# Kernel optimization log

Measured on AMD Instinct MI355X. Metric: run time of the kernel, lower is better.

## Reference

```python
import jax, jax.numpy as jnp
import numpy as np


def setup_inputs() -> dict:
    key = jax.random.key(0)
    ks = jax.random.split(key, 18)
    B, T, L, C = 16, 512, 50, 7
    H = 512
    s = 0.05
    inp = {
        "phone_data": jax.random.normal(ks[0], (B, T, L, C), jnp.float32),
        "h0": jax.random.normal(ks[1], (B, H), jnp.float32),
        "conv1_w": jax.random.normal(ks[2], (128, 7, 11), jnp.float32) * s,
        "conv1_b": jax.random.normal(ks[3], (128,), jnp.float32) * s,
        "conv2_w": jax.random.normal(ks[4], (256, 128, 9), jnp.float32) * s,
        "conv2_b": jax.random.normal(ks[5], (256,), jnp.float32) * s,
        "fc1_w": jax.random.normal(ks[6], (1024, 1536), jnp.float32) * s,
        "fc1_b": jax.random.normal(ks[7], (1024,), jnp.float32) * s,
        "fc2_w": jax.random.normal(ks[8], (512, 1024), jnp.float32) * s,
        "fc2_b": jax.random.normal(ks[9], (512,), jnp.float32) * s,
        "gru_wih": jax.random.normal(ks[10], (3 * H, H), jnp.float32) * s,
        "gru_whh": jax.random.normal(ks[11], (3 * H, H), jnp.float32) * s,
        "gru_bih": jax.random.normal(ks[12], (3 * H,), jnp.float32) * s,
        "gru_bhh": jax.random.normal(ks[13], (3 * H,), jnp.float32) * s,
        "fc3_w": jax.random.normal(ks[14], (1, H), jnp.float32) * s,
        "fc3_b": jax.random.normal(ks[15], (1,), jnp.float32) * s,
    }
    return inp


def reference(phone_data, h0, conv1_w, conv1_b, conv2_w, conv2_b,
              fc1_w, fc1_b, fc2_w, fc2_b,
              gru_wih, gru_whh, gru_bih, gru_bhh, fc3_w, fc3_b):
    B, T, L, C = phone_data.shape
    N = B * T
    # ---- batched CNN + FC feature extractor (independent per frame) ----
    x = phone_data.reshape(N, L, C).transpose(0, 2, 1)  # [N, 7, 50]
    y = jax.lax.conv_general_dilated(
        x, conv1_w, (1,), 'VALID',
        dimension_numbers=('NCH', 'OIH', 'NCH')) + conv1_b[None, :, None]  # [N,128,40]
    y = y.reshape(N, 128, 20, 2).max(-1)  # maxpool k=2,s=2 -> [N,128,20]
    y = jax.lax.conv_general_dilated(
        y, conv2_w, (1,), 'VALID',
        dimension_numbers=('NCH', 'OIH', 'NCH')) + conv2_b[None, :, None]  # [N,256,12]
    y = y.reshape(N, 256, 6, 2).max(-1)  # [N,256,6]
    feat = y.reshape(N, 1536)            # Flatten(0): channel-major, matches torch
    feat = feat @ fc1_w.T + fc1_b        # [N,1024]
    feat = feat @ fc2_w.T + fc2_b        # [N,512]
    feat = feat.reshape(B, T, 512)

    # ---- sequential GRUCell recurrence (PyTorch GRUCell math) ----
    def cell(h, x_t):
        gi = x_t @ gru_wih.T + gru_bih   # [B, 3H]
        gh = h @ gru_whh.T + gru_bhh     # [B, 3H]
        ir, iz, in_ = jnp.split(gi, 3, axis=-1)
        hr, hz, hn = jnp.split(gh, 3, axis=-1)
        r = jax.nn.sigmoid(ir + hr)
        z = jax.nn.sigmoid(iz + hz)
        n = jnp.tanh(in_ + r * hn)
        h_new = (1 - z) * n + z * h
        # original code calls hx.detach() every step
        h_new = jax.lax.stop_gradient(h_new)
        return h_new, h_new

    _, hs = jax.lax.scan(cell, h0, feat.transpose(1, 0, 2))  # hs: [T,B,512]
    out = hs @ fc3_w.T + fc3_b  # [T,B,1]
    return out.transpose(1, 0, 2)  # [B,T,1]
```

## Files before the change

### kernel.cpp

```cpp
#include <hip/hip_runtime.h>
#include <hip/hip_bf16.h>
#include <math.h>
#include <stdint.h>

typedef __attribute__((ext_vector_type(8))) short short8;
typedef __attribute__((ext_vector_type(4))) float f32x4;
typedef __attribute__((ext_vector_type(4))) unsigned int uint4v;

#define T_ 512

__device__ __forceinline__ unsigned short bf16rn(float f) {
  union { float f; unsigned u; } x; x.f = f;
  unsigned r = x.u + 0x7FFF + ((x.u >> 16) & 1);
  return (unsigned short)(r >> 16);
}

__device__ __forceinline__ void gload16(const void* gsrc, void* ldst) {
  __builtin_amdgcn_global_load_lds(
      (const __attribute__((address_space(1))) unsigned int*)gsrc,
      (__attribute__((address_space(3))) unsigned int*)ldst, 16, 0, 0);
}

__device__ __forceinline__ void wg_barrier() {
  __builtin_amdgcn_sched_barrier(0);
  asm volatile("s_waitcnt lgkmcnt(0)" ::: "memory");
  __builtin_amdgcn_sched_barrier(0);
  __builtin_amdgcn_s_barrier();
  __builtin_amdgcn_sched_barrier(0);
}

__global__ __launch_bounds__(256) void conv1_kernel(
    const float* __restrict__ phone, const float* __restrict__ w1,
    const float* __restrict__ b1, ushort* __restrict__ out1b) {
  __shared__ float ws[128 * 77];
  __shared__ float bs[128];
  __shared__ float xs[8][7][52];
  const int tid = threadIdx.x;
  const int n0 = blockIdx.x * 8;
  for (int idx = tid; idx < 9856; idx += 256) ws[idx] = w1[idx];
  if (tid < 128) bs[tid] = b1[tid];
  for (int idx = tid; idx < 2800; idx += 256) {
    int fi = idx / 350, r = idx - fi * 350;
    int ll = r / 7, c = r - ll * 7;
    xs[fi][c][ll] = phone[(size_t)(n0 + fi) * 350 + r];
  }
  __syncthreads();

  const int o = tid >> 1, ph = tid & 1;
  const float* wo = ws + o * 77;
  const float bb = bs[o];
  for (int fi = 0; fi < 8; ++fi) {
    float acc0[10], acc1[10];
#pragma unroll
    for (int q = 0; q < 10; ++q) { acc0[q] = 0.f; acc1[q] = 0.f; }
    for (int i = 0; i < 7; ++i) {
      float wr[11];
#pragma unroll
      for (int k = 0; k < 11; ++k) wr[k] = wo[i * 11 + k];
#pragma unroll
      for (int q = 0; q < 10; ++q) {
        int p = ph * 10 + q;
        int base = 2 * p;
        float xv[12];
#pragma unroll
        for (int j = 0; j < 12; ++j) xv[j] = xs[fi][i][base + j];
        float s0 = 0.f, s1 = 0.f;
#pragma unroll
        for (int k = 0; k < 11; ++k) {
          s0 += xv[k] * wr[k];
          s1 += xv[k + 1] * wr[k];
        }
        acc0[q] += s0;
        acc1[q] += s1;
      }
    }
#pragma unroll
    for (int q = 0; q < 10; ++q) {
      int p = ph * 10 + q;
      out1b[((size_t)(n0 + fi) * 128 + o) * 20 + p] =
          bf16rn(fmaxf(acc0[q], acc1[q]) + bb);
    }
  }
}

__global__ __launch_bounds__(256) void f32_to_bf16(
    const float* __restrict__ src, ushort* __restrict__ dst, int n4) {
  int i = blockIdx.x * 256 + threadIdx.x;
  if (i < n4) {
    float4 v = ((const float4*)src)[i];
    ushort4 o;
    o.x = bf16rn(v.x); o.y = bf16rn(v.y); o.z = bf16rn(v.z); o.w = bf16rn(v.w);
    ((ushort4*)dst)[i] = o;
  }
}

__global__ __launch_bounds__(256) void stage_h0(
    const float* __restrict__ h0, unsigned long long* __restrict__ hxt) {
  const int tid = threadIdx.x;
  const int b = tid >> 4, x = tid & 15;
#pragma unroll
  for (int q = 0; q < 16; ++q) {
    int d = (x + q * 16) * 2;
    int s = d >> 5, fqq = (d >> 3) & 3, k = (d & 7) >> 1;
    int lane = b | (fqq << 4);
    float2 h2 = *(const float2*)(h0 + (size_t)b * 512 + d);
    unsigned pk = (unsigned)bf16rn(h2.x) | ((unsigned)bf16rn(h2.y) << 16);
    hxt[((size_t)s * 64 + lane) * 4 + k] = (unsigned long long)pk;
  }
}

template <int AM, int EM>
__global__ __launch_bounds__(256) void gemm_bf16(
    const ushort* __restrict__ A, const ushort* __restrict__ W,
    const float* __restrict__ bias, void* __restrict__ Cout,
    int K, int lda, int ldc) {
  __shared__ ushort As[128 * 64];
  __shared__ ushort Bs[128 * 64];
  __shared__ ushort tbl[1152];
  const int tid = threadIdx.x;
  const int l = tid & 63, wv = tid >> 6;
  const int wr = wv >> 1, wc = wv & 1;
  const int fr = l & 15, fq = l >> 4;
  const int bm0 = blockIdx.x * 128, bn0 = blockIdx.y * 128;

  if (AM == 1) {
    for (int idx = tid; idx < 1152; idx += 256) {
      int i2 = idx / 9, kp = idx - i2 * 9;
      tbl[idx] = (ushort)(i2 * 20 + kp);
    }
    __syncthreads();
  }

  f32x4 acc[4][4];
#pragma unroll
  for (int mi = 0; mi < 4; ++mi)
#pragma unroll
    for (int ni = 0; ni < 4; ++ni) acc[mi][ni] = (f32x4)0.f;

  const int pr8 = l >> 3;
  const int pc = l & 7;
  const int nkt = K >> 6;
  for (int kt = 0; kt < nkt; ++kt) {
    const int k0 = kt << 6;
#pragma unroll
    for (int i = 0; i < 4; ++i) {
      int q = wv * 4 + i;
      int prow = q * 8 + pr8;
      int lc = pc ^ (prow & 7);
      gload16(W + (size_t)(bn0 + prow) * K + k0 + lc * 8, &Bs[q * 512]);
    }
    if (AM == 0) {
#pragma unroll
      for (int i = 0; i < 4; ++i) {
        int q = wv * 4 + i;
        int prow = q * 8 + pr8;
        int lc = pc ^ (prow & 7);
        gload16(A + (size_t)(bm0 + prow) * lda + k0 + lc * 8, &As[q * 512]);
      }
    } else {
#pragma unroll
      for (int q = 0; q < 16; ++q) {
        int idx = tid + q * 256;
        int row = idx >> 5, c0 = (idx & 31) * 2;
        int m = bm0 + row;
        int n = m / 12, pos = m - n * 12;
        int kk = k0 + c0;
        const ushort* an = A + (size_t)n * 2560 + pos;
        uint e0 = an[tbl[kk]];
        uint e1 = an[tbl[kk + 1]];
        *(uint*)&As[row * 64 + (((c0 >> 3) ^ (row & 7)) << 3) + (c0 & 7)] =
            e0 | (e1 << 16);
      }
    }
    __syncthreads();
#pragma unroll
    for (int ks = 0; ks < 2; ++ks) {
      short8 af[4], bfr[4];
#pragma unroll
      for (int mi = 0; mi < 4; ++mi) {
        int row = wr * 64 + mi * 16 + fr;
        af[mi] = *(const short8*)&As[row * 64 + (((ks * 4 + fq) ^ (row & 7)) << 3)];
      }
#pragma unroll
      for (int ni = 0; ni < 4; ++ni) {
        int row = wc * 64 + ni * 16 + fr;
        bfr[ni] = *(const short8*)&Bs[row * 64 + (((ks * 4 + fq) ^ (row & 7)) << 3)];
      }
#pragma unroll
      for (int mi = 0; mi < 4; ++mi)
#pragma unroll
        for (int ni = 0; ni < 4; ++ni)
          acc[mi][ni] = __builtin_amdgcn_mfma_f32_16x16x32_bf16(
              af[mi], bfr[ni], acc[mi][ni], 0, 0, 0);
    }
    __syncthreads();
  }

#pragma unroll
  for (int ni = 0; ni < 4; ++ni) {
    int col = bn0 + wc * 64 + ni * 16 + fr;
    float bv = bias[col];
#pragma unroll
    for (int mi = 0; mi < 4; ++mi) {
      int mbase = bm0 + wr * 64 + mi * 16 + fq * 4;
      if (EM == 0) {
        ushort* C = (ushort*)Cout;
#pragma unroll
        for (int j = 0; j < 4; ++j)
          C[(size_t)(mbase + j) * ldc + col] = bf16rn(acc[mi][ni][j] + bv);
      } else if (EM == 1) {
        ushort* C = (ushort*)Cout;
#pragma unroll
        for (int j = 0; j < 4; j += 2) {
          int m = mbase + j;
          int n = m / 12, pos = m - n * 12;
          float v = fmaxf(acc[mi][ni][j], acc[mi][ni][j + 1]) + bv;
          C[(size_t)n * 1536 + col * 6 + (pos >> 1)] = bf16rn(v);
        }
      } else {
        float* C = (float*)Cout;
#pragma unroll
        for (int j = 0; j < 4; ++j) {
          int m = mbase + j;
          int b = m >> 9, tt = m & 511;
          C[((size_t)tt * 16 + b) * 1536 + col] = acc[mi][ni][j] + bv;
        }
      }
    }
  }
}

__global__ __launch_bounds__(384) void gru_persistent(
    const float* __restrict__ h0, const float* __restrict__ gi,
    const float* __restrict__ whh, const float* __restrict__ bhh,
    float* __restrict__ hsbuf, unsigned long long* __restrict__ hxt) {
  __shared__ float gh_lds[6 * 256];
  __shared__ unsigned afl[16 * 64 * 4];
  const int tid = threadIdx.x;
  const int w = blockIdx.x;
  const int l = tid & 63, v = tid >> 6;
  const int fr = l & 15, fq = l >> 4;
  const int g = v >> 1, half = v & 1;
  const int o = g * 512 + w * 32 + half * 16 + fr;

  short8 bfrag[16];
#pragma unroll
  for (int s = 0; s < 16; ++s) {
    const float* wp = whh + (size_t)o * 512 + s * 32 + fq * 8;
    float4 w0 = *(const float4*)wp;
    float4 w1 = *(const float4*)(wp + 4);
    short8 bb;
    bb[0] = (short)bf16rn(w0.x); bb[1] = (short)bf16rn(w0.y);
    bb[2] = (short)bf16rn(w0.z); bb[3] = (short)bf16rn(w0.w);
    bb[4] = (short)bf16rn(w1.x); bb[5] = (short)bf16rn(w1.y);
    bb[6] = (short)bf16rn(w1.z); bb[7] = (short)bf16rn(w1.w);
    bfrag[s] = bb;
  }
  const float bo = bhh[o];

  const int b = tid >> 4, jp = tid & 15, jl = jp * 2;
  const bool gthr = (tid < 256);
  const int pt = tid - 256;
  float hA = 0.f, hB = 0.f;
  float giC0 = 0.f, giC1 = 0.f, giC2 = 0.f, giC3 = 0.f, giC4 = 0.f, giC5 = 0.f;
  float giN0 = 0.f, giN1 = 0.f, giN2 = 0.f, giN3 = 0.f, giN4 = 0.f, giN5 = 0.f;
  if (gthr) {
    float2 h2 = *(const float2*)(h0 + (size_t)b * 512 + w * 32 + jl);
    hA = h2.x; hB = h2.y;
    const float* g0 = gi + (size_t)b * 1536 + w * 32 + jl;
    float2 r0 = *(const float2*)(g0);
    float2 r1 = *(const float2*)(g0 + 512);
    float2 r2 = *(const float2*)(g0 + 1024);
    giC0 = r0.x; giC3 = r0.y; giC1 = r1.x; giC4 = r1.y; giC2 = r2.x; giC5 = r2.y;
    const float* g1 = gi + (size_t)(16 + b) * 1536 + w * 32 + jl;
    float2 s0 = *(const float2*)(g1);
    float2 s1 = *(const float2*)(g1 + 512);
    float2 s2 = *(const float2*)(g1 + 1024);
    giN0 = s0.x; giN3 = s0.y; giN1 = s1.x; giN4 = s1.y; giN2 = s2.x; giN5 = s2.y;
  }

  if (!gthr) {
    const unsigned long long* base = hxt + pt * 2;
    uint4v r[16];
    for (;;) {
#pragma unroll
      for (int m = 0; m < 16; ++m)
        asm volatile("global_load_dwordx4 %0, %1, off sc0 sc1"
                     : "=v"(r[m]) : "v"(base + m * 256));
      asm volatile("s_waitcnt vmcnt(0)" ::: "memory");
      __builtin_amdgcn_sched_barrier(0);
      bool ok = true;
#pragma unroll
      for (int m = 0; m < 16; ++m)
        ok = ok & (r[m].y == 0u) & (r[m].w == 0u);
      if (ok) break;
    }
#pragma unroll
    for (int m = 0; m < 16; ++m)
      *(uint2*)&afl[pt * 2 + m * 256] = make_uint2(r[m].x, r[m].z);
  }
  wg_barrier();

  for (int t = 0; t < T_; ++t) {
    f32x4 a0 = (f32x4)0.f, a1 = (f32x4)0.f, a2 = (f32x4)0.f, a3 = (f32x4)0.f;
#pragma unroll
    for (int s = 0; s < 4; ++s) {
      union { uint4v u; short8 s8; } c0, c1, c2, c3;
      c0.u = *(const uint4v*)&afl[((4 * s + 0) * 64 + l) * 4];
      c1.u = *(const uint4v*)&afl[((4 * s + 1) * 64 + l) * 4];
      c2.u = *(const uint4v*)&afl[((4 * s + 2) * 64 + l) * 4];
      c3.u = *(const uint4v*)&afl[((4 * s + 3) * 64 + l) * 4];
      a0 = __builtin_amdgcn_mfma_f32_16x16x32_bf16(c0.s8, bfrag[4 * s + 0], a0, 0, 0, 0);
      a1 = __builtin_amdgcn_mfma_f32_16x16x32_bf16(c1.s8, bfrag[4 * s + 1], a1, 0, 0, 0);
      a2 = __builtin_amdgcn_mfma_f32_16x16x32_bf16(c2.s8, bfrag[4 * s + 2], a2, 0, 0, 0);
      a3 = __builtin_amdgcn_mfma_f32_16x16x32_bf16(c3.s8, bfrag[4 * s + 3], a3, 0, 0, 0);
    }
#pragma unroll
    for (int j = 0; j < 4; ++j)
      gh_lds[v * 256 + (fq * 4 + j) * 16 + fr] = a0[j] + a1[j] + a2[j] + a3[j] + bo;
    wg_barrier();

    if (gthr) {
      const int hh = jl >> 4, c = jl & 15;
      float2 rr = *(const float2*)&gh_lds[(0 + hh) * 256 + b * 16 + c];
      float2 zz = *(const float2*)&gh_lds[(2 + hh) * 256 + b * 16 + c];
      float2 nn = *(const float2*)&gh_lds[(4 + hh) * 256 + b * 16 + c];
      float rgA = __builtin_amdgcn_rcpf(1.f + __expf(-(giC0 + rr.x)));
      float rgB = __builtin_amdgcn_rcpf(1.f + __expf(-(giC3 + rr.y)));
      float zgA = __builtin_amdgcn_rcpf(1.f + __expf(-(giC1 + zz.x)));
      float zgB = __builtin_amdgcn_rcpf(1.f + __expf(-(giC4 + zz.y)));
      float eA = __expf(2.f * (giC2 + rgA * nn.x));
      float eB = __expf(2.f * (giC5 + rgB * nn.y));
      float ngA = 1.f - 2.f * __builtin_amdgcn_rcpf(eA + 1.f);
      float ngB = 1.f - 2.f * __builtin_amdgcn_rcpf(eB + 1.f);
      hA = (1.f - zgA) * ngA + zgA * hA;
      hB = (1.f - zgB) * ngB + zgB * hB;
      if (t + 1 < T_) {
        unsigned pk = (unsigned)bf16rn(hA) | ((unsigned)bf16rn(hB) << 16);
        unsigned long long payload =
            (unsigned long long)pk | ((unsigned long long)(unsigned)(t + 1) << 32);
        unsigned long long* dst =
            hxt + (((size_t)((t + 1) & 1) * 16 + w) * 64 + (b | ((jp >> 2) << 4))) * 4 +
            (jp & 3);
        __hip_atomic_store(dst, payload, __ATOMIC_RELAXED, __HIP_MEMORY_SCOPE_AGENT);
      }
      *(float2*)(hsbuf + ((size_t)t * 16 + b) * 512 + w * 32 + jl) =
          make_float2(hA, hB);
      giC0 = giN0; giC1 = giN1; giC2 = giN2;
      giC3 = giN3; giC4 = giN4; giC5 = giN5;
      if (t + 2 < T_) {
        const float* gb = gi + ((size_t)(t + 2) * 16 + b) * 1536 + w * 32 + jl;
        float2 r0 = *(const float2*)(gb);
        float2 r1 = *(const float2*)(gb + 512);
        float2 r2 = *(const float2*)(gb + 1024);
        giN0 = r0.x; giN3 = r0.y; giN1 = r1.x; giN4 = r1.y; giN2 = r2.x; giN5 = r2.y;
      }
    } else if (t + 1 < T_) {
      const unsigned long long* base =
          hxt + (size_t)((t + 1) & 1) * 4096 + pt * 2;
      const unsigned tag = (unsigned)(t + 1);
      uint4v r[16];
      for (;;) {
#pragma unroll
        for (int m = 0; m < 16; ++m)
          asm volatile("global_load_dwordx4 %0, %1, off sc0 sc1"
                       : "=v"(r[m]) : "v"(base + m * 256));
        asm volatile("s_waitcnt vmcnt(0)" ::: "memory");
        __builtin_amdgcn_sched_barrier(0);
        bool ok = true;
#pragma unroll
        for (int m = 0; m < 16; ++m)
          ok = ok & (r[m].y == tag) & (r[m].w == tag);
        if (ok) break;
      }
#pragma unroll
      for (int m = 0; m < 16; ++m)
        *(uint2*)&afl[pt * 2 + m * 256] = make_uint2(r[m].x, r[m].z);
    }
    wg_barrier();
  }
}

__global__ __launch_bounds__(256) void fc3_kernel(
    const float* __restrict__ hs, const float* __restrict__ w3,
    const float* __restrict__ b3, float* __restrict__ out) {
  __shared__ float w[512];
  const int tid = threadIdx.x;
  w[tid] = w3[tid];
  w[tid + 256] = w3[tid + 256];
  __syncthreads();
  const int gidx = blockIdx.x * 256 + tid;
  const int b = gidx >> 9, t = gidx & 511;
  const float4* hr = (const float4*)(hs + ((size_t)t * 16 + b) * 512);
  const float4* wr = (const float4*)w;
  float acc = 0.f;
#pragma unroll 8
  for (int kc = 0; kc < 128; ++kc) {
    float4 h = hr[kc], ww = wr[kc];
    acc += h.x * ww.x + h.y * ww.y + h.z * ww.z + h.w * ww.w;
  }
  out[gidx] = acc + b3[0];
}

extern "C" void kernel_launch(void* const* d_in, const int* in_sizes, int n_in,
                              void* d_out, int out_size, void* d_ws,
                              size_t ws_size, hipStream_t stream) {
  const float* phone = (const float*)d_in[0];
  const float* h0    = (const float*)d_in[1];
  const float* w1    = (const float*)d_in[2];
  const float* b1    = (const float*)d_in[3];
  const float* w2    = (const float*)d_in[4];
  const float* b2    = (const float*)d_in[5];
  const float* fc1w  = (const float*)d_in[6];
  const float* fc1b  = (const float*)d_in[7];
  const float* fc2w  = (const float*)d_in[8];
  const float* fc2b  = (const float*)d_in[9];
  const float* wih   = (const float*)d_in[10];
  const float* whh   = (const float*)d_in[11];
  const float* bih   = (const float*)d_in[12];
  const float* bhh   = (const float*)d_in[13];
  const float* w3    = (const float*)d_in[14];
  const float* b3    = (const float*)d_in[15];
  float* out = (float*)d_out;

  char* ws = (char*)d_ws;
  ushort* out1b = (ushort*)(ws + 0);
  ushort* feat2 = (ushort*)(ws + 41943040);
  ushort* feat3 = (ushort*)(ws + 67108864);
  ushort* feat4 = (ushort*)(ws + 83886080);
  float*  gibuf = (float*) (ws + 92274688);
  float*  hsbuf = (float*) (ws + 142606336);
  ushort* w2b   = (ushort*)(ws + 159383552);
  ushort* fc1wb = (ushort*)(ws + 159973376);
  ushort* fc2wb = (ushort*)(ws + 163119104);
  ushort* wihb  = (ushort*)(ws + 164167680);
  unsigned long long* hxt = (unsigned long long*)(ws + 67108864);

  f32_to_bf16<<<288, 256, 0, stream>>>(w2, w2b, 73728);
  f32_to_bf16<<<1536, 256, 0, stream>>>(fc1w, fc1wb, 393216);
  f32_to_bf16<<<512, 256, 0, stream>>>(fc2w, fc2wb, 131072);
  f32_to_bf16<<<768, 256, 0, stream>>>(wih, wihb, 196608);

  conv1_kernel<<<1024, 256, 0, stream>>>(phone, w1, b1, out1b);
  gemm_bf16<1, 1><<<dim3(768, 2), 256, 0, stream>>>(out1b, w2b, b2, feat2, 1152, 0, 0);
  gemm_bf16<0, 0><<<dim3(64, 8), 256, 0, stream>>>(feat2, fc1wb, fc1b, feat3, 1536, 1536, 1024);
  gemm_bf16<0, 0><<<dim3(64, 4), 256, 0, stream>>>(feat3, fc2wb, fc2b, feat4, 1024, 1024, 512);
  gemm_bf16<0, 2><<<dim3(64, 12), 256, 0, stream>>>(feat4, wihb, bih, gibuf, 512, 512, 1536);

  hipMemsetAsync(hxt, 0, 65536, stream);
  stage_h0<<<1, 256, 0, stream>>>(h0, hxt);
  gru_persistent<<<16, 384, 0, stream>>>(h0, gibuf, whh, bhh, hsbuf, hxt);

  fc3_kernel<<<32, 256, 0, stream>>>(hsbuf, w3, b3, out);
}
```

Before: 1.700 ms.

## Split GRU batch into two independent 8-batch groups of persistent blocks

The persistent GRU kernel is repartitioned so each block handles 8 batch rows and 64 hidden units instead of 16 rows and 32 units. The batch is split into two independent groups with separate hidden-state exchange buffers, so each group synchronises only among its own 8 blocks. Each wave now computes two output tiles with 16 weight fragments each. The aim is to cut per-step cross-block polling traffic and the number of participants in each exchange. The cost is double the weight registers per wave, and half the MFMA rows are wasted because only 8 of the 16 batch rows are live.

```diff
diff --git a/kernel.cpp b/kernel.cpp
--- a/kernel.cpp
+++ b/kernel.cpp
@@ -97,15 +97,17 @@
 __global__ __launch_bounds__(256) void stage_h0(
     const float* __restrict__ h0, unsigned long long* __restrict__ hxt) {
   const int tid = threadIdx.x;
-  const int b = tid >> 4, x = tid & 15;
-#pragma unroll
-  for (int q = 0; q < 16; ++q) {
-    int d = (x + q * 16) * 2;
-    int s = d >> 5, fqq = (d >> 3) & 3, k = (d & 7) >> 1;
-    int lane = b | (fqq << 4);
+#pragma unroll
+  for (int k = 0; k < 16; ++k) {
+    int idx = tid + k * 256;
+    int g = idx >> 11, rem = idx & 2047;
+    int s = rem >> 7, w_i = rem & 127;
+    int b8 = (w_i >> 2) & 7, fqk = w_i >> 5, p2 = w_i & 3;
+    int b = g * 8 + b8;
+    int d = s * 32 + fqk * 8 + p2 * 2;
     float2 h2 = *(const float2*)(h0 + (size_t)b * 512 + d);
     unsigned pk = (unsigned)bf16rn(h2.x) | ((unsigned)bf16rn(h2.y) << 16);
-    hxt[((size_t)s * 64 + lane) * 4 + k] = (unsigned long long)pk;
+    hxt[(size_t)g * 4096 + s * 128 + w_i] = (unsigned long long)pk;
   }
 }
 
@@ -234,45 +236,54 @@
     const float* __restrict__ h0, const float* __restrict__ gi,
     const float* __restrict__ whh, const float* __restrict__ bhh,
     float* __restrict__ hsbuf, unsigned long long* __restrict__ hxt) {
-  __shared__ float gh_lds[6 * 256];
+  __shared__ float gh_lds[12 * 256];
   __shared__ unsigned afl[16 * 64 * 4];
   const int tid = threadIdx.x;
-  const int w = blockIdx.x;
+  const int g = blockIdx.x >> 3, wp = blockIdx.x & 7;
   const int l = tid & 63, v = tid >> 6;
   const int fr = l & 15, fq = l >> 4;
-  const int g = v >> 1, half = v & 1;
-  const int o = g * 512 + w * 32 + half * 16 + fr;
-
-  short8 bfrag[16];
+  unsigned long long* hxg = hxt + (size_t)g * 4096;
+
+  const int t0 = 2 * v, t1 = 2 * v + 1;
+  const int o0 = (t0 >> 2) * 512 + wp * 64 + (t0 & 3) * 16 + fr;
+  const int o1 = (t1 >> 2) * 512 + wp * 64 + (t1 & 3) * 16 + fr;
+  short8 bf0[16], bf1[16];
 #pragma unroll
   for (int s = 0; s < 16; ++s) {
-    const float* wp = whh + (size_t)o * 512 + s * 32 + fq * 8;
-    float4 w0 = *(const float4*)wp;
-    float4 w1 = *(const float4*)(wp + 4);
-    short8 bb;
-    bb[0] = (short)bf16rn(w0.x); bb[1] = (short)bf16rn(w0.y);
-    bb[2] = (short)bf16rn(w0.z); bb[3] = (short)bf16rn(w0.w);
-    bb[4] = (short)bf16rn(w1.x); bb[5] = (short)bf16rn(w1.y);
-    bb[6] = (short)bf16rn(w1.z); bb[7] = (short)bf16rn(w1.w);
-    bfrag[s] = bb;
-  }
-  const float bo = bhh[o];
-
-  const int b = tid >> 4, jp = tid & 15, jl = jp * 2;
+    const float* wp0 = whh + (size_t)o0 * 512 + s * 32 + fq * 8;
+    const float* wp1 = whh + (size_t)o1 * 512 + s * 32 + fq * 8;
+    float4 a0 = *(const float4*)wp0, a1 = *(const float4*)(wp0 + 4);
+    float4 c0 = *(const float4*)wp1, c1 = *(const float4*)(wp1 + 4);
+    short8 x, y;
+    x[0] = (short)bf16rn(a0.x); x[1] = (short)bf16rn(a0.y);
+    x[2] = (short)bf16rn(a0.z); x[3] = (short)bf16rn(a0.w);
+    x[4] = (short)bf16rn(a1.x); x[5] = (short)bf16rn(a1.y);
+    x[6] = (short)bf16rn(a1.z); x[7] = (short)bf16rn(a1.w);
+    y[0] = (short)bf16rn(c0.x); y[1] = (short)bf16rn(c0.y);
+    y[2] = (short)bf16rn(c0.z); y[3] = (short)bf16rn(c0.w);
+    y[4] = (short)bf16rn(c1.x); y[5] = (short)bf16rn(c1.y);
+    y[6] = (short)bf16rn(c1.z); y[7] = (short)bf16rn(c1.w);
+    bf0[s] = x; bf1[s] = y;
+  }
+  const float bo0 = bhh[o0], bo1 = bhh[o1];
+
+  const int b8 = tid >> 5, jp = tid & 31, jl = jp * 2;
   const bool gthr = (tid < 256);
   const int pt = tid - 256;
+  const int bglob = g * 8 + b8;
+  const int jglob = wp * 64 + jl;
   float hA = 0.f, hB = 0.f;
   float giC0 = 0.f, giC1 = 0.f, giC2 = 0.f, giC3 = 0.f, giC4 = 0.f, giC5 = 0.f;
   float giN0 = 0.f, giN1 = 0.f, giN2 = 0.f, giN3 = 0.f, giN4 = 0.f, giN5 = 0.f;
   if (gthr) {
-    float2 h2 = *(const float2*)(h0 + (size_t)b * 512 + w * 32 + jl);
+    float2 h2 = *(const float2*)(h0 + (size_t)bglob * 512 + jglob);
     hA = h2.x; hB = h2.y;
-    const float* g0 = gi + (size_t)b * 1536 + w * 32 + jl;
+    const float* g0 = gi + (size_t)bglob * 1536 + jglob;
     float2 r0 = *(const float2*)(g0);
     float2 r1 = *(const float2*)(g0 + 512);
     float2 r2 = *(const float2*)(g0 + 1024);
     giC0 = r0.x; giC3 = r0.y; giC1 = r1.x; giC4 = r1.y; giC2 = r2.x; giC5 = r2.y;
-    const float* g1 = gi + (size_t)(16 + b) * 1536 + w * 32 + jl;
+    const float* g1 = gi + (size_t)(16 + bglob) * 1536 + jglob;
     float2 s0 = *(const float2*)(g1);
     float2 s1 = *(const float2*)(g1 + 512);
     float2 s2 = *(const float2*)(g1 + 1024);
@@ -280,51 +291,56 @@
   }
 
   if (!gthr) {
-    const unsigned long long* base = hxt + pt * 2;
-    uint4v r[16];
+    const int ps = pt >> 3;
+    const int pw0 = (pt & 7) * 2;
+    const unsigned long long* base = hxg + ps * 128;
+    uint4v r[8];
     for (;;) {
 #pragma unroll
-      for (int m = 0; m < 16; ++m)
+      for (int q = 0; q < 8; ++q)
         asm volatile("global_load_dwordx4 %0, %1, off sc0 sc1"
-                     : "=v"(r[m]) : "v"(base + m * 256));
+                     : "=v"(r[q]) : "v"(base + pw0 + q * 16));
       asm volatile("s_waitcnt vmcnt(0)" ::: "memory");
       __builtin_amdgcn_sched_barrier(0);
       bool ok = true;
 #pragma unroll
-      for (int m = 0; m < 16; ++m)
-        ok = ok & (r[m].y == 0u) & (r[m].w == 0u);
+      for (int q = 0; q < 8; ++q)
+        ok = ok & (r[q].y == 0u) & (r[q].w == 0u);
       if (ok) break;
     }
 #pragma unroll
-    for (int m = 0; m < 16; ++m)
-      *(uint2*)&afl[pt * 2 + m * 256] = make_uint2(r[m].x, r[m].z);
+    for (int q = 0; q < 8; ++q) {
+      int w_i = pw0 + q * 16;
+      int lane = ((w_i >> 2) & 7) + 16 * (w_i >> 5);
+      *(uint2*)&afl[(ps * 64 + lane) * 4 + (w_i & 3)] = make_uint2(r[q].x, r[q].z);
+    }
   }
   wg_barrier();
 
   for (int t = 0; t < T_; ++t) {
-    f32x4 a0 = (f32x4)0.f, a1 = (f32x4)0.f, a2 = (f32x4)0.f, a3 = (f32x4)0.f;
-#pragma unroll
-    for (int s = 0; s < 4; ++s) {
-      union { uint4v u; short8 s8; } c0, c1, c2, c3;
-      c0.u = *(const uint4v*)&afl[((4 * s + 0) * 64 + l) * 4];
-      c1.u = *(const uint4v*)&afl[((4 * s + 1) * 64 + l) * 4];
-      c2.u = *(const uint4v*)&afl[((4 * s + 2) * 64 + l) * 4];
-      c3.u = *(const uint4v*)&afl[((4 * s + 3) * 64 + l) * 4];
-      a0 = __builtin_amdgcn_mfma_f32_16x16x32_bf16(c0.s8, bfrag[4 * s + 0], a0, 0, 0, 0);
-      a1 = __builtin_amdgcn_mfma_f32_16x16x32_bf16(c1.s8, bfrag[4 * s + 1], a1, 0, 0, 0);
-      a2 = __builtin_amdgcn_mfma_f32_16x16x32_bf16(c2.s8, bfrag[4 * s + 2], a2, 0, 0, 0);
-      a3 = __builtin_amdgcn_mfma_f32_16x16x32_bf16(c3.s8, bfrag[4 * s + 3], a3, 0, 0, 0);
-    }
-#pragma unroll
-    for (int j = 0; j < 4; ++j)
-      gh_lds[v * 256 + (fq * 4 + j) * 16 + fr] = a0[j] + a1[j] + a2[j] + a3[j] + bo;
+    f32x4 e0 = (f32x4)0.f, q0 = (f32x4)0.f, e1 = (f32x4)0.f, q1 = (f32x4)0.f;
+#pragma unroll
+    for (int s = 0; s < 16; s += 2) {
+      union { uint4v u; short8 s8; } ca, cb;
+      ca.u = *(const uint4v*)&afl[((s + 0) * 64 + l) * 4];
+      cb.u = *(const uint4v*)&afl[((s + 1) * 64 + l) * 4];
+      e0 = __builtin_amdgcn_mfma_f32_16x16x32_bf16(ca.s8, bf0[s], e0, 0, 0, 0);
+      q0 = __builtin_amdgcn_mfma_f32_16x16x32_bf16(cb.s8, bf0[s + 1], q0, 0, 0, 0);
+      e1 = __builtin_amdgcn_mfma_f32_16x16x32_bf16(ca.s8, bf1[s], e1, 0, 0, 0);
+      q1 = __builtin_amdgcn_mfma_f32_16x16x32_bf16(cb.s8, bf1[s + 1], q1, 0, 0, 0);
+    }
+#pragma unroll
+    for (int j = 0; j < 4; ++j) {
+      gh_lds[t0 * 256 + (fq * 4 + j) * 16 + fr] = e0[j] + q0[j] + bo0;
+      gh_lds[t1 * 256 + (fq * 4 + j) * 16 + fr] = e1[j] + q1[j] + bo1;
+    }
     wg_barrier();
 
     if (gthr) {
       const int hh = jl >> 4, c = jl & 15;
-      float2 rr = *(const float2*)&gh_lds[(0 + hh) * 256 + b * 16 + c];
-      float2 zz = *(const float2*)&gh_lds[(2 + hh) * 256 + b * 16 + c];
-      float2 nn = *(const float2*)&gh_lds[(4 + hh) * 256 + b * 16 + c];
+      float2 rr = *(const float2*)&gh_lds[(0 + hh) * 256 + b8 * 16 + c];
+      float2 zz = *(const float2*)&gh_lds[(4 + hh) * 256 + b8 * 16 + c];
+      float2 nn = *(const float2*)&gh_lds[(8 + hh) * 256 + b8 * 16 + c];
       float rgA = __builtin_amdgcn_rcpf(1.f + __expf(-(giC0 + rr.x)));
       float rgB = __builtin_amdgcn_rcpf(1.f + __expf(-(giC3 + rr.y)));
       float zgA = __builtin_amdgcn_rcpf(1.f + __expf(-(giC1 + zz.x)));
@@ -339,43 +355,48 @@
         unsigned pk = (unsigned)bf16rn(hA) | ((unsigned)bf16rn(hB) << 16);
         unsigned long long payload =
             (unsigned long long)pk | ((unsigned long long)(unsigned)(t + 1) << 32);
-        unsigned long long* dst =
-            hxt + (((size_t)((t + 1) & 1) * 16 + w) * 64 + (b | ((jp >> 2) << 4))) * 4 +
-            (jp & 3);
-        __hip_atomic_store(dst, payload, __ATOMIC_RELAXED, __HIP_MEMORY_SCOPE_AGENT);
-      }
-      *(float2*)(hsbuf + ((size_t)t * 16 + b) * 512 + w * 32 + jl) =
+        int s = wp * 2 + (jl >> 5);
+        int w_i = (((jl & 31) >> 3) * 8 + b8) * 4 + (jp & 3);
+        __hip_atomic_store(hxg + ((t + 1) & 1) * 2048 + s * 128 + w_i, payload,
+                           __ATOMIC_RELAXED, __HIP_MEMORY_SCOPE_AGENT);
+      }
+      *(float2*)(hsbuf + ((size_t)t * 16 + bglob) * 512 + jglob) =
           make_float2(hA, hB);
       giC0 = giN0; giC1 = giN1; giC2 = giN2;
       giC3 = giN3; giC4 = giN4; giC5 = giN5;
       if (t + 2 < T_) {
-        const float* gb = gi + ((size_t)(t + 2) * 16 + b) * 1536 + w * 32 + jl;
+        const float* gb = gi + ((size_t)(t + 2) * 16 + bglob) * 1536 + jglob;
         float2 r0 = *(const float2*)(gb);
         float2 r1 = *(const float2*)(gb + 512);
         float2 r2 = *(const float2*)(gb + 1024);
         giN0 = r0.x; giN3 = r0.y; giN1 = r1.x; giN4 = r1.y; giN2 = r2.x; giN5 = r2.y;
       }
     } else if (t + 1 < T_) {
+      const int ps = pt >> 3;
+      const int pw0 = (pt & 7) * 2;
       const unsigned long long* base =
-          hxt + (size_t)((t + 1) & 1) * 4096 + pt * 2;
+          hxg + ((t + 1) & 1) * 2048 + ps * 128;
       const unsigned tag = (unsigned)(t + 1);
-      uint4v r[16];
+      uint4v r[8];
       for (;;) {
 #pragma unroll
-        for (int m = 0; m < 16; ++m)
+        for (int q = 0; q < 8; ++q)
           asm volatile("global_load_dwordx4 %0, %1, off sc0 sc1"
-                       : "=v"(r[m]) : "v"(base + m * 256));
+                       : "=v"(r[q]) : "v"(base + pw0 + q * 16));
         asm volatile("s_waitcnt vmcnt(0)" ::: "memory");
         __builtin_amdgcn_sched_barrier(0);
         bool ok = true;
 #pragma unroll
-        for (int m = 0; m < 16; ++m)
-          ok = ok & (r[m].y == tag) & (r[m].w == tag);
+        for (int q = 0; q < 8; ++q)
+          ok = ok & (r[q].y == tag) & (r[q].w == tag);
         if (ok) break;
       }
 #pragma unroll
-      for (int m = 0; m < 16; ++m)
-        *(uint2*)&afl[pt * 2 + m * 256] = make_uint2(r[m].x, r[m].z);
+      for (int q = 0; q < 8; ++q) {
+        int w_i = pw0 + q * 16;
+        int lane = ((w_i >> 2) & 7) + 16 * (w_i >> 5);
+        *(uint2*)&afl[(ps * 64 + lane) * 4 + (w_i & 3)] = make_uint2(r[q].x, r[q].z);
+      }
     }
     wg_barrier();
   }
```

Result: faster. 1.495 ms (-12.0%).
